# Optimization experiments

Measured on AMD Instinct MI355X. Metric: run time of the kernel, lower is better.

## Reference

```python
import jax, jax.numpy as jnp
import numpy as np

N_USERS = 60000
N_ITEMS = 30000
N_NODES = N_USERS + N_ITEMS
D = 64
L = 2


def _norm_adj(edge_index):
    # symmetrize: A_idx = [e, e.flip(0)]
    src = jnp.concatenate([edge_index[0], edge_index[1]])
    dst = jnp.concatenate([edge_index[1], edge_index[0]])
    ones = jnp.ones_like(src, dtype=jnp.float32)
    deg = jax.ops.segment_sum(ones, src, num_segments=N_NODES)
    deg = jnp.clip(deg, 1.0, None)
    val = jax.lax.rsqrt(deg[src]) * jax.lax.rsqrt(deg[dst])
    return src, dst, val


def _spmm(src, dst, val, x):
    # out[i] = sum_{(i,j) in E} val_ij * x[j]
    return jax.ops.segment_sum(val[:, None] * x[dst], src, num_segments=N_NODES)


def setup_inputs() -> dict:
    key = jax.random.key(0)
    ks = jax.random.split(key, 20)
    s = 0.02
    inp = {
        'x_txt': jax.random.normal(ks[0], (N_ITEMS, 768), jnp.float32),
        'x_img': jax.random.normal(ks[1], (N_ITEMS, 512), jnp.float32),
        'x_struct': jax.random.normal(ks[2], (N_ITEMS, 128), jnp.float32),
        'user_emb': jax.random.normal(ks[3], (3, N_USERS, D), jnp.float32) * s,
        'W_txt': jax.random.normal(ks[4], (3, 768, D), jnp.float32) * s,
        'b_txt': jax.random.normal(ks[5], (3, D), jnp.float32) * s,
        'W_img': jax.random.normal(ks[6], (3, 512, D), jnp.float32) * s,
        'b_img': jax.random.normal(ks[7], (3, D), jnp.float32) * s,
        'W_st': jax.random.normal(ks[8], (3, 128, D), jnp.float32) * s,
        'b_st': jax.random.normal(ks[9], (3, D), jnp.float32) * s,
        'Wu1': jax.random.normal(ks[10], (3 * D, 128), jnp.float32) * s,
        'bu1': jax.random.normal(ks[11], (128,), jnp.float32) * s,
        'Wu2': jax.random.normal(ks[12], (128, 3), jnp.float32) * s,
        'bu2': jax.random.normal(ks[13], (3,), jnp.float32) * s,
        'Wi1': jax.random.normal(ks[14], (3 * D, 128), jnp.float32) * s,
        'bi1': jax.random.normal(ks[15], (128,), jnp.float32) * s,
        'Wi2': jax.random.normal(ks[16], (128, 3), jnp.float32) * s,
        'bi2': jax.random.normal(ks[17], (3,), jnp.float32) * s,
        'edge_index': jax.random.randint(ks[18], (2, 500000), 0, N_NODES, jnp.int64),
    }
    return inp


def reference(x_txt, x_img, x_struct, user_emb, W_txt, b_txt, W_img, b_img,
              W_st, b_st, Wu1, bu1, Wu2, bu2, Wi1, bi1, Wi2, bi2, edge_index):
    src, dst, val = _norm_adj(edge_index)

    # item embeddings for all 3 branches at once: [n_items, 3, d]
    i0 = (jnp.einsum('nt,btd->nbd', x_txt, W_txt) + b_txt
          + jnp.einsum('nt,btd->nbd', x_img, W_img) + b_img
          + jnp.einsum('nt,btd->nbd', x_struct, W_st) + b_st)
    u0 = jnp.transpose(user_emb, (1, 0, 2))  # [n_users, 3, d]
    x = jnp.concatenate([u0, i0], axis=0).reshape(N_NODES, 3 * D)

    out = x
    for _ in range(L):
        x = _spmm(src, dst, val, x)
        out = out + x
    out = out / (L + 1)

    stack = out.reshape(N_NODES, 3, D)
    U_stack, I_stack = stack[:N_USERS], stack[N_USERS:]
    U_cat = U_stack.reshape(N_USERS, 3 * D)
    I_cat = I_stack.reshape(N_ITEMS, 3 * D)

    a_u = jax.nn.softmax(jax.nn.relu(U_cat @ Wu1 + bu1) @ Wu2 + bu2, axis=-1)
    a_i = jax.nn.softmax(jax.nn.relu(I_cat @ Wi1 + bi1) @ Wi2 + bi2, axis=-1)

    U = jnp.einsum('nb,nbd->nd', a_u, U_stack)
    I = jnp.einsum('nb,nbd->nd', a_i, I_stack)
    return jnp.concatenate([U, I], axis=0)  # [N_NODES, d]
```

## Files before the change

### kernel.cpp

```cpp
#include <hip/hip_runtime.h>
#include <math.h>

#define N_USERS 60000
#define N_ITEMS 30000
#define N_NODES 90000
#define DD 64
#define FF 192
#define FH 96
#define KK_TOT 1408
#define E_UND 500000
#define E_DIR 1000000
#define SCAN_NBLK 88

typedef __attribute__((ext_vector_type(8))) __bf16 bf16x8;
typedef __attribute__((ext_vector_type(8))) unsigned short u16x8;
typedef __attribute__((ext_vector_type(4))) float f32x4;

__device__ __forceinline__ unsigned short f2bf(float f) {
    unsigned int u = __float_as_uint(f);
    unsigned int r = (u + 0x7FFFu + ((u >> 16) & 1u)) >> 16;
    return (unsigned short)r;
}
__device__ __forceinline__ float bf_lo(unsigned int x) { return __uint_as_float(x << 16); }
__device__ __forceinline__ float bf_hi(unsigned int x) { return __uint_as_float(x & 0xFFFF0000u); }
__device__ __forceinline__ float bf2f(unsigned short x) {
    return __uint_as_float((unsigned int)x << 16);
}
__device__ __forceinline__ unsigned int pack2(float a, float b) {
    return ((unsigned int)f2bf(b) << 16) | (unsigned int)f2bf(a);
}

__global__ void k_mode(const int* __restrict__ ei, int* __restrict__ mode) {
    __shared__ int any;
    if (threadIdx.x == 0) any = 0;
    __syncthreads();
    if (ei[2 * threadIdx.x + 1] != 0) atomicOr(&any, 1);
    __syncthreads();
    if (threadIdx.x == 0) mode[0] = (any == 0) ? 1 : 0;
}

__device__ __forceinline__ void load_pair(const int* __restrict__ ei, int md, int u,
                                          int& a, int& b) {
    if (md) { a = ei[2 * u]; b = ei[2 * (E_UND + u)]; }
    else    { a = ei[u];     b = ei[E_UND + u]; }
}

__global__ void k_deg(const int* __restrict__ ei, const int* __restrict__ mode,
                      int* __restrict__ deg) {
    int i = blockIdx.x * 256 + threadIdx.x;
    if (i >= E_UND) return;
    int md = mode[0];
    int a, b;
    load_pair(ei, md, i, a, b);
    atomicAdd(&deg[a], 1);
    atomicAdd(&deg[b], 1);
}

__global__ __launch_bounds__(1024) void k_scan1(const int* __restrict__ deg,
                                                int* __restrict__ offs,
                                                int* __restrict__ bsum) {
    __shared__ int tmp[1024];
    int b = blockIdx.x, t = threadIdx.x;
    int i = b * 1024 + t;
    int v = (i < N_NODES) ? deg[i] : 0;
    tmp[t] = v;
    __syncthreads();
    for (int off = 1; off < 1024; off <<= 1) {
        int add = (t >= off) ? tmp[t - off] : 0;
        __syncthreads();
        tmp[t] += add;
        __syncthreads();
    }
    offs[i] = tmp[t] - v;
    if (t == 1023) bsum[b] = tmp[t];
}

__global__ void k_scan2(const int* __restrict__ bsum, int* __restrict__ bscan) {
    if (threadIdx.x == 0) {
        int run = 0;
        for (int b = 0; b < SCAN_NBLK; b++) { bscan[b] = run; run += bsum[b]; }
    }
}

__global__ void k_scan3(const int* __restrict__ deg, int* __restrict__ offs,
                        const int* __restrict__ bscan, int* __restrict__ cursor,
                        float* __restrict__ rsq) {
    int i = blockIdx.x * 256 + threadIdx.x;
    if (i >= N_NODES) return;
    int o = offs[i] + bscan[i >> 10];
    offs[i] = o;
    cursor[i] = o;
    int dg = deg[i];
    if (dg < 1) dg = 1;
    rsq[i] = rsqrtf((float)dg);
}

__global__ void k_fill(const int* __restrict__ ei, const int* __restrict__ mode,
                       int* __restrict__ cursor, const float* __restrict__ rsq,
                       int* __restrict__ edst, float* __restrict__ eval) {
    int i = blockIdx.x * 256 + threadIdx.x;
    if (i >= E_DIR) return;
    int md = mode[0];
    int u = (i < E_UND) ? i : i - E_UND;
    int a, b;
    load_pair(ei, md, u, a, b);
    int s, d;
    if (i < E_UND) { s = a; d = b; } else { s = b; d = a; }
    int slot = atomicAdd(&cursor[s], 1);
    edst[slot] = d;
    eval[slot] = rsq[s] * rsq[d];
}

__global__ void k_users(const float* __restrict__ ue, unsigned short* __restrict__ Xbs) {
    int idx = blockIdx.x * 256 + threadIdx.x;
    if (idx >= N_USERS * FF) return;
    int n = idx / FF;
    int r = idx - n * FF;
    int b = r >> 6, d = r & 63;
    Xbs[idx] = f2bf(ue[((size_t)b * N_USERS + n) * DD + d]);
}

__global__ void k_cvt_w(const float* __restrict__ Wt, const float* __restrict__ Wi,
                        const float* __restrict__ Wst, unsigned short* __restrict__ Wtb) {
    int idx = blockIdx.x * 256 + threadIdx.x;
    if (idx >= FF * KK_TOT) return;
    int n = idx / KK_TOT;
    int k = idx - n * KK_TOT;
    int b = n >> 6, d = n & 63;
    float v;
    if (k < 768)       v = Wt [((size_t)b * 768 + k) * 64 + d];
    else if (k < 1280) v = Wi [((size_t)b * 512 + (k - 768)) * 64 + d];
    else               v = Wst[((size_t)b * 128 + (k - 1280)) * 64 + d];
    Wtb[idx] = f2bf(v);
}

__global__ void k_cvt_w1(const float* __restrict__ Wu1, const float* __restrict__ Wi1,
                         unsigned short* __restrict__ W1Tu,
                         unsigned short* __restrict__ W1Ti) {
    int idx = blockIdx.x * 256 + threadIdx.x;
    if (idx >= 128 * FF) return;
    int n = idx / FF;
    int k = idx - n * FF;
    W1Tu[idx] = f2bf(Wu1[(size_t)k * 128 + n]);
    W1Ti[idx] = f2bf(Wi1[(size_t)k * 128 + n]);
}

#define BM 64
#define BNH 96
#define BK 64
#define LDK 72

__global__ __launch_bounds__(256) void k_item_gemm_mfma3(
    const float* __restrict__ xt, const float* __restrict__ xi, const float* __restrict__ xs,
    const unsigned short* __restrict__ Wtb,
    const float* __restrict__ bt, const float* __restrict__ bi, const float* __restrict__ bst,
    unsigned short* __restrict__ Xbs) {
    __shared__ unsigned short Ash[BM * LDK];
    __shared__ unsigned short Bsh[BNH * LDK];
    const int tid  = threadIdx.x;
    const int wave = tid >> 6;
    const int lane = tid & 63;
    const int row0 = (blockIdx.x >> 1) * BM;
    const int n0   = (blockIdx.x & 1) * BNH;

    f32x4 acc[6];
#pragma unroll
    for (int tn = 0; tn < 6; tn++) acc[tn] = (f32x4){0.f, 0.f, 0.f, 0.f};

    const int l16  = lane & 15;
    const int quad = lane >> 4;

    for (int k0 = 0; k0 < KK_TOT; k0 += BK) {
#pragma unroll
        for (int i = 0; i < 2; i++) {
            int id = tid + i * 256;
            int r = id >> 3;
            int c = (id & 7) << 3;
            int gr = row0 + r;
            int gk = k0 + c;
            float4 v0 = make_float4(0.f, 0.f, 0.f, 0.f);
            float4 v1 = v0;
            if (gr < N_ITEMS) {
                const float* src;
                int kl;
                if (gk < 768)       { src = xt + (size_t)gr * 768; kl = gk; }
                else if (gk < 1280) { src = xi + (size_t)gr * 512; kl = gk - 768; }
                else                { src = xs + (size_t)gr * 128; kl = gk - 1280; }
                v0 = *(const float4*)(src + kl);
                v1 = *(const float4*)(src + kl + 4);
            }
            u16x8 pk;
            pk[0] = f2bf(v0.x); pk[1] = f2bf(v0.y); pk[2] = f2bf(v0.z); pk[3] = f2bf(v0.w);
            pk[4] = f2bf(v1.x); pk[5] = f2bf(v1.y); pk[6] = f2bf(v1.z); pk[7] = f2bf(v1.w);
            *(u16x8*)(&Ash[r * LDK + c]) = pk;
        }
#pragma unroll
        for (int i = 0; i < 3; i++) {
            int id = tid + i * 256;
            int r = id >> 3;
            int c = (id & 7) << 3;
            *(u16x8*)(&Bsh[r * LDK + c]) =
                *(const u16x8*)(&Wtb[(size_t)(n0 + r) * KK_TOT + k0 + c]);
        }
        __syncthreads();
#pragma unroll
        for (int kk = 0; kk < BK; kk += 32) {
            bf16x8 af = *(const bf16x8*)(&Ash[(wave * 16 + l16) * LDK + kk + quad * 8]);
#pragma unroll
            for (int tn = 0; tn < 6; tn++) {
                bf16x8 bfr = *(const bf16x8*)(&Bsh[(tn * 16 + l16) * LDK + kk + quad * 8]);
                acc[tn] = __builtin_amdgcn_mfma_f32_16x16x32_bf16(af, bfr, acc[tn], 0, 0, 0);
            }
        }
        __syncthreads();
    }

#pragma unroll
    for (int tn = 0; tn < 6; tn++) {
        int n = n0 + tn * 16 + l16;
        int b = n >> 6, d = n & 63;
        float bias = bt[b * 64 + d] + bi[b * 64 + d] + bst[b * 64 + d];
#pragma unroll
        for (int r = 0; r < 4; r++) {
            int row = row0 + wave * 16 + quad * 4 + r;
            if (row < N_ITEMS) {
                Xbs[(size_t)(N_USERS + row) * FF + n] = f2bf(acc[tn][r] + bias);
            }
        }
    }
}

__global__ __launch_bounds__(192) void k_spmm_bf(const unsigned int* __restrict__ Xb,
                                                 unsigned int* __restrict__ Yb,
                                                 const int* __restrict__ offs,
                                                 const int* __restrict__ deg,
                                                 const int* __restrict__ edst,
                                                 const float* __restrict__ eval) {
    int t = threadIdx.x;
    int half = (t >= FH) ? 1 : 0;
    int c = t - half * FH;
    int n = blockIdx.x * 2 + half;
    int start = offs[n];
    int dg = deg[n];
    const int* ed = edst + start;
    const float* ev = eval + start;
    float a0 = 0.f, a1 = 0.f;
    for (int j = 0; j < dg; j += 4) {
        int last = dg - 1;
        int j1 = (j + 1 < dg) ? j + 1 : last;
        int j2 = (j + 2 < dg) ? j + 2 : last;
        int j3 = (j + 3 < dg) ? j + 3 : last;
        int d0 = ed[j], d1 = ed[j1], d2 = ed[j2], d3 = ed[j3];
        float v0 = ev[j];
        float v1 = (j + 1 < dg) ? ev[j1] : 0.f;
        float v2 = (j + 2 < dg) ? ev[j2] : 0.f;
        float v3 = (j + 3 < dg) ? ev[j3] : 0.f;
        unsigned int x0 = Xb[(size_t)d0 * FH + c];
        unsigned int x1 = Xb[(size_t)d1 * FH + c];
        unsigned int x2 = Xb[(size_t)d2 * FH + c];
        unsigned int x3 = Xb[(size_t)d3 * FH + c];
        a0 = fmaf(v0, bf_lo(x0), a0); a1 = fmaf(v0, bf_hi(x0), a1);
        a0 = fmaf(v1, bf_lo(x1), a0); a1 = fmaf(v1, bf_hi(x1), a1);
        a0 = fmaf(v2, bf_lo(x2), a0); a1 = fmaf(v2, bf_hi(x2), a1);
        a0 = fmaf(v3, bf_lo(x3), a0); a1 = fmaf(v3, bf_hi(x3), a1);
    }
    Yb[(size_t)n * FH + c] = pack2(a0, a1);
}

#define LDA 200

__global__ __launch_bounds__(256) void k_attn_mfma(
    const unsigned int* __restrict__ X0,
    const unsigned int* __restrict__ X1,
    const unsigned int* __restrict__ X2,
    const unsigned short* __restrict__ W1T,
    const float* __restrict__ B1,
    const float* __restrict__ W2,
    const float* __restrict__ B2,
    float* __restrict__ out,
    int node_base, int n_rows) {
    __shared__ unsigned short Atile[64 * LDA];
    __shared__ float aws[64][4];
    const int tid  = threadIdx.x;
    const int wave = tid >> 6;
    const int lane = tid & 63;
    const int row0 = blockIdx.x * 64;
    const float inv3 = 1.f / 3.f;

#pragma unroll
    for (int i = 0; i < 6; i++) {
        int id = tid + i * 256;
        int r = id / 24;
        int q = id - r * 24;
        u16x8 pk;
        if (row0 + r < n_rows) {
            size_t base = (size_t)(node_base + row0 + r) * FH + q * 4;
            uint4 a = *(const uint4*)(X0 + base);
            uint4 b = *(const uint4*)(X1 + base);
            uint4 c = *(const uint4*)(X2 + base);
            pk[0] = f2bf((bf_lo(a.x) + bf_lo(b.x) + bf_lo(c.x)) * inv3);
            pk[1] = f2bf((bf_hi(a.x) + bf_hi(b.x) + bf_hi(c.x)) * inv3);
            pk[2] = f2bf((bf_lo(a.y) + bf_lo(b.y) + bf_lo(c.y)) * inv3);
            pk[3] = f2bf((bf_hi(a.y) + bf_hi(b.y) + bf_hi(c.y)) * inv3);
            pk[4] = f2bf((bf_lo(a.z) + bf_lo(b.z) + bf_lo(c.z)) * inv3);
            pk[5] = f2bf((bf_hi(a.z) + bf_hi(b.z) + bf_hi(c.z)) * inv3);
            pk[6] = f2bf((bf_lo(a.w) + bf_lo(b.w) + bf_lo(c.w)) * inv3);
            pk[7] = f2bf((bf_hi(a.w) + bf_hi(b.w) + bf_hi(c.w)) * inv3);
        } else {
            pk = (u16x8){0, 0, 0, 0, 0, 0, 0, 0};
        }
        *(u16x8*)(&Atile[r * LDA + q * 8]) = pk;
    }
    __syncthreads();

    f32x4 acc[8];
#pragma unroll
    for (int tn = 0; tn < 8; tn++) acc[tn] = (f32x4){0.f, 0.f, 0.f, 0.f};
    const int l16 = lane & 15;
    const int quad = lane >> 4;
#pragma unroll
    for (int kk = 0; kk < FF; kk += 32) {
        bf16x8 af = *(const bf16x8*)(&Atile[(wave * 16 + l16) * LDA + kk + quad * 8]);
#pragma unroll
        for (int tn = 0; tn < 8; tn++) {
            bf16x8 bf = *(const bf16x8*)(&W1T[(size_t)(tn * 16 + l16) * FF + kk + quad * 8]);
            acc[tn] = __builtin_amdgcn_mfma_f32_16x16x32_bf16(af, bf, acc[tn], 0, 0, 0);
        }
    }

    float pl[4][3];
#pragma unroll
    for (int r = 0; r < 4; r++) { pl[r][0] = 0.f; pl[r][1] = 0.f; pl[r][2] = 0.f; }
#pragma unroll
    for (int tn = 0; tn < 8; tn++) {
        int col = tn * 16 + l16;
        float b1v = B1[col];
        float w0 = W2[col * 3 + 0], w1 = W2[col * 3 + 1], w2v = W2[col * 3 + 2];
#pragma unroll
        for (int r = 0; r < 4; r++) {
            float h = fmaxf(acc[tn][r] + b1v, 0.f);
            pl[r][0] = fmaf(h, w0, pl[r][0]);
            pl[r][1] = fmaf(h, w1, pl[r][1]);
            pl[r][2] = fmaf(h, w2v, pl[r][2]);
        }
    }
#pragma unroll
    for (int m = 1; m <= 8; m <<= 1) {
#pragma unroll
        for (int r = 0; r < 4; r++) {
            pl[r][0] += __shfl_xor(pl[r][0], m, 64);
            pl[r][1] += __shfl_xor(pl[r][1], m, 64);
            pl[r][2] += __shfl_xor(pl[r][2], m, 64);
        }
    }
    float b20 = B2[0], b21 = B2[1], b22 = B2[2];
    if (l16 == 0) {
#pragma unroll
        for (int r = 0; r < 4; r++) {
            float l0 = pl[r][0] + b20, l1 = pl[r][1] + b21, l2 = pl[r][2] + b22;
            float mx = fmaxf(l0, fmaxf(l1, l2));
            float e0 = __expf(l0 - mx), e1 = __expf(l1 - mx), e2 = __expf(l2 - mx);
            float inv = 1.f / (e0 + e1 + e2);
            int rr = wave * 16 + quad * 4 + r;
            aws[rr][0] = e0 * inv; aws[rr][1] = e1 * inv; aws[rr][2] = e2 * inv;
        }
    }
    __syncthreads();

#pragma unroll
    for (int i = 0; i < 16; i++) {
        int flat = tid + i * 256;
        int r = flat >> 6, d = flat & 63;
        if (row0 + r < n_rows) {
            float a0 = aws[r][0], a1 = aws[r][1], a2 = aws[r][2];
            const unsigned short* Ar = &Atile[r * LDA];
            float v = a0 * bf2f(Ar[d]) + a1 * bf2f(Ar[64 + d]) + a2 * bf2f(Ar[128 + d]);
            out[(size_t)(node_base + row0 + r) * DD + d] = v;
        }
    }
}

extern "C" void kernel_launch(void* const* d_in, const int* in_sizes, int n_in,
                              void* d_out, int out_size, void* d_ws, size_t ws_size,
                              hipStream_t stream) {
    (void)in_sizes; (void)n_in; (void)out_size; (void)ws_size;
    const float* x_txt    = (const float*)d_in[0];
    const float* x_img    = (const float*)d_in[1];
    const float* x_struct = (const float*)d_in[2];
    const float* user_emb = (const float*)d_in[3];
    const float* W_txt    = (const float*)d_in[4];
    const float* b_txt    = (const float*)d_in[5];
    const float* W_img    = (const float*)d_in[6];
    const float* b_img    = (const float*)d_in[7];
    const float* W_st     = (const float*)d_in[8];
    const float* b_st     = (const float*)d_in[9];
    const float* Wu1      = (const float*)d_in[10];
    const float* bu1      = (const float*)d_in[11];
    const float* Wu2      = (const float*)d_in[12];
    const float* bu2      = (const float*)d_in[13];
    const float* Wi1      = (const float*)d_in[14];
    const float* bi1      = (const float*)d_in[15];
    const float* Wi2      = (const float*)d_in[16];
    const float* bi2      = (const float*)d_in[17];
    const int*   ei       = (const int*)d_in[18];
    float* out = (float*)d_out;

    char* base = (char*)d_ws;
    size_t off = 0;
    auto take = [&](size_t bytes) -> void* {
        void* p = base + off;
        off += (bytes + 255) & ~(size_t)255;
        return p;
    };
    unsigned int* Xb0  = (unsigned int*)take((size_t)N_NODES * FH * 4);
    unsigned int* Yb   = (unsigned int*)take((size_t)N_NODES * FH * 4);
    unsigned int* Zb   = (unsigned int*)take((size_t)N_NODES * FH * 4);
    int* deg    = (int*)take((size_t)N_NODES * 4);
    int* offs   = (int*)take((size_t)SCAN_NBLK * 1024 * 4);
    int* cursor = (int*)take((size_t)N_NODES * 4);
    int* bsum   = (int*)take((size_t)SCAN_NBLK * 4);
    int* bscan  = (int*)take((size_t)SCAN_NBLK * 4);
    float* rsq  = (float*)take((size_t)N_NODES * 4);
    int* edst   = (int*)take((size_t)E_DIR * 4);
    float* eval = (float*)take((size_t)E_DIR * 4);
    int* mode   = (int*)take(256);
    unsigned short* Wtb  = (unsigned short*)take((size_t)FF * KK_TOT * 2);
    unsigned short* W1Tu = (unsigned short*)take((size_t)128 * FF * 2);
    unsigned short* W1Ti = (unsigned short*)take((size_t)128 * FF * 2);

    hipMemsetAsync(deg, 0, (size_t)N_NODES * 4, stream);

    k_mode<<<1, 256, 0, stream>>>(ei, mode);
    k_deg<<<(E_UND + 255) / 256, 256, 0, stream>>>(ei, mode, deg);
    k_scan1<<<SCAN_NBLK, 1024, 0, stream>>>(deg, offs, bsum);
    k_scan2<<<1, 64, 0, stream>>>(bsum, bscan);
    k_scan3<<<(N_NODES + 255) / 256, 256, 0, stream>>>(deg, offs, bscan, cursor, rsq);
    k_fill<<<(E_DIR + 255) / 256, 256, 0, stream>>>(ei, mode, cursor, rsq, edst, eval);

    k_users<<<(N_USERS * FF + 255) / 256, 256, 0, stream>>>(user_emb,
                                                            (unsigned short*)Xb0);
    k_cvt_w<<<(FF * KK_TOT + 255) / 256, 256, 0, stream>>>(W_txt, W_img, W_st, Wtb);
    k_cvt_w1<<<(128 * FF + 255) / 256, 256, 0, stream>>>(Wu1, Wi1, W1Tu, W1Ti);
    k_item_gemm_mfma3<<<((N_ITEMS + BM - 1) / BM) * 2, 256, 0, stream>>>(
        x_txt, x_img, x_struct, Wtb, b_txt, b_img, b_st, (unsigned short*)Xb0);

    k_spmm_bf<<<N_NODES / 2, 192, 0, stream>>>(Xb0, Yb, offs, deg, edst, eval);
    k_spmm_bf<<<N_NODES / 2, 192, 0, stream>>>(Yb, Zb, offs, deg, edst, eval);

    k_attn_mfma<<<(N_USERS + 63) / 64, 256, 0, stream>>>(
        Xb0, Yb, Zb, W1Tu, bu1, Wu2, bu2, out, 0, N_USERS);
    k_attn_mfma<<<(N_ITEMS + 63) / 64, 256, 0, stream>>>(
        Xb0, Yb, Zb, W1Ti, bi1, Wi2, bi2, out, N_USERS, N_ITEMS);
}
```

Baseline: 619.7 us.

## Double-buffer item GEMM tiles with register prefetch of next K slice

The item-embedding GEMM now keeps two LDS buffers and loads the next K tile's global data into registers while the current tile's MFMAs run. This drops one barrier per iteration and hides global load latency behind compute. Out-of-range rows are clamped to the last row instead of zero-filled, and their outputs are masked at store. The cost is doubled LDS use and more live registers, which may lower occupancy.

```diff
diff --git a/kernel.cpp b/kernel.cpp
--- a/kernel.cpp
+++ b/kernel.cpp
@@ -155,14 +155,43 @@
     const unsigned short* __restrict__ Wtb,
     const float* __restrict__ bt, const float* __restrict__ bi, const float* __restrict__ bst,
     unsigned short* __restrict__ Xbs) {
-    __shared__ unsigned short Ash[BM * LDK];
-    __shared__ unsigned short Bsh[BNH * LDK];
+    __shared__ unsigned short Ash[2][BM * LDK];
+    __shared__ unsigned short Bsh[2][BNH * LDK];
     const int tid  = threadIdx.x;
     const int wave = tid >> 6;
     const int lane = tid & 63;
     const int row0 = (blockIdx.x >> 1) * BM;
     const int n0   = (blockIdx.x & 1) * BNH;
 
+    const int sr = tid >> 3;
+    const int sc = (tid & 7) << 3;
+
+    int gr0 = row0 + sr;        if (gr0 >= N_ITEMS) gr0 = N_ITEMS - 1;
+    int gr1 = row0 + sr + 32;   if (gr1 >= N_ITEMS) gr1 = N_ITEMS - 1;
+
+    const size_t bbase = (size_t)(n0 + sr) * KK_TOT + sc;
+
+    float4 pa[2][2];
+    u16x8  pb[3];
+
+    auto issue = [&](int k0) {
+        int kl = k0 + sc;
+        const float *s0, *s1;
+        if (kl < 768)       { s0 = xt + (size_t)gr0 * 768 + kl;
+                              s1 = xt + (size_t)gr1 * 768 + kl; }
+        else if (kl < 1280) { s0 = xi + (size_t)gr0 * 512 + (kl - 768);
+                              s1 = xi + (size_t)gr1 * 512 + (kl - 768); }
+        else                { s0 = xs + (size_t)gr0 * 128 + (kl - 1280);
+                              s1 = xs + (size_t)gr1 * 128 + (kl - 1280); }
+        pa[0][0] = *(const float4*)(s0);
+        pa[0][1] = *(const float4*)(s0 + 4);
+        pa[1][0] = *(const float4*)(s1);
+        pa[1][1] = *(const float4*)(s1 + 4);
+        pb[0] = *(const u16x8*)(&Wtb[bbase + k0]);
+        pb[1] = *(const u16x8*)(&Wtb[bbase + k0 + (size_t)32 * KK_TOT]);
+        pb[2] = *(const u16x8*)(&Wtb[bbase + k0 + (size_t)64 * KK_TOT]);
+    };
+
     f32x4 acc[6];
 #pragma unroll
     for (int tn = 0; tn < 6; tn++) acc[tn] = (f32x4){0.f, 0.f, 0.f, 0.f};
@@ -170,49 +199,36 @@
     const int l16  = lane & 15;
     const int quad = lane >> 4;
 
+    issue(0);
+    int cur = 0;
     for (int k0 = 0; k0 < KK_TOT; k0 += BK) {
 #pragma unroll
         for (int i = 0; i < 2; i++) {
-            int id = tid + i * 256;
-            int r = id >> 3;
-            int c = (id & 7) << 3;
-            int gr = row0 + r;
-            int gk = k0 + c;
-            float4 v0 = make_float4(0.f, 0.f, 0.f, 0.f);
-            float4 v1 = v0;
-            if (gr < N_ITEMS) {
-                const float* src;
-                int kl;
-                if (gk < 768)       { src = xt + (size_t)gr * 768; kl = gk; }
-                else if (gk < 1280) { src = xi + (size_t)gr * 512; kl = gk - 768; }
-                else                { src = xs + (size_t)gr * 128; kl = gk - 1280; }
-                v0 = *(const float4*)(src + kl);
-                v1 = *(const float4*)(src + kl + 4);
-            }
             u16x8 pk;
-            pk[0] = f2bf(v0.x); pk[1] = f2bf(v0.y); pk[2] = f2bf(v0.z); pk[3] = f2bf(v0.w);
-            pk[4] = f2bf(v1.x); pk[5] = f2bf(v1.y); pk[6] = f2bf(v1.z); pk[7] = f2bf(v1.w);
-            *(u16x8*)(&Ash[r * LDK + c]) = pk;
-        }
-#pragma unroll
-        for (int i = 0; i < 3; i++) {
-            int id = tid + i * 256;
-            int r = id >> 3;
-            int c = (id & 7) << 3;
-            *(u16x8*)(&Bsh[r * LDK + c]) =
-                *(const u16x8*)(&Wtb[(size_t)(n0 + r) * KK_TOT + k0 + c]);
-        }
+            pk[0] = f2bf(pa[i][0].x); pk[1] = f2bf(pa[i][0].y);
+            pk[2] = f2bf(pa[i][0].z); pk[3] = f2bf(pa[i][0].w);
+            pk[4] = f2bf(pa[i][1].x); pk[5] = f2bf(pa[i][1].y);
+            pk[6] = f2bf(pa[i][1].z); pk[7] = f2bf(pa[i][1].w);
+            *(u16x8*)(&Ash[cur][(sr + i * 32) * LDK + sc]) = pk;
+        }
+#pragma unroll
+        for (int i = 0; i < 3; i++)
+            *(u16x8*)(&Bsh[cur][(sr + i * 32) * LDK + sc]) = pb[i];
+
+        if (k0 + BK < KK_TOT) issue(k0 + BK);
+
         __syncthreads();
+
 #pragma unroll
         for (int kk = 0; kk < BK; kk += 32) {
-            bf16x8 af = *(const bf16x8*)(&Ash[(wave * 16 + l16) * LDK + kk + quad * 8]);
+            bf16x8 af = *(const bf16x8*)(&Ash[cur][(wave * 16 + l16) * LDK + kk + quad * 8]);
 #pragma unroll
             for (int tn = 0; tn < 6; tn++) {
-                bf16x8 bfr = *(const bf16x8*)(&Bsh[(tn * 16 + l16) * LDK + kk + quad * 8]);
+                bf16x8 bfr = *(const bf16x8*)(&Bsh[cur][(tn * 16 + l16) * LDK + kk + quad * 8]);
                 acc[tn] = __builtin_amdgcn_mfma_f32_16x16x32_bf16(af, bfr, acc[tn], 0, 0, 0);
             }
         }
-        __syncthreads();
+        cur ^= 1;
     }
 
 #pragma unroll
```

Result: no change. 610.6 us (-1.5%).

## Double-buffer item GEMM with direct global-to-LDS loads and full-N tiles

Applied to the files above, without the earlier changes.

Rewrites the item projection GEMM so each 512-thread block computes all 192 output columns for 64 rows, instead of splitting N across two blocks. That halves the reads of the fp32 activation inputs. Tiles are copied straight into LDS with global_load_lds, using XOR-swizzled layouts and double buffering, so the next K tile loads while MFMAs run on the current one. The fp32-to-bf16 conversion moves from the staging path to fragment-read time. The cost is more LDS per block, repeated conversions, and hand-placed waitcnt and barrier synchronisation that must be exactly right.

```diff
diff --git a/kernel.cpp b/kernel.cpp
--- a/kernel.cpp
+++ b/kernel.cpp
@@ -15,6 +15,18 @@
 typedef __attribute__((ext_vector_type(8))) __bf16 bf16x8;
 typedef __attribute__((ext_vector_type(8))) unsigned short u16x8;
 typedef __attribute__((ext_vector_type(4))) float f32x4;
+
+typedef __attribute__((address_space(1))) const void gvoid;
+typedef __attribute__((address_space(3))) void svoid;
+
+__device__ __forceinline__ void gll16(const void* g, void* l) {
+    __builtin_amdgcn_global_load_lds((gvoid*)g, (svoid*)l, 16, 0, 0);
+}
+__device__ __forceinline__ void fence_bar() {
+    asm volatile("" ::: "memory");
+    __builtin_amdgcn_s_barrier();
+    asm volatile("" ::: "memory");
+}
 
 __device__ __forceinline__ unsigned short f2bf(float f) {
     unsigned int u = __float_as_uint(f);
@@ -146,83 +158,100 @@
 }
 
 #define BM 64
-#define BNH 96
 #define BK 64
-#define LDK 72
-
-__global__ __launch_bounds__(256) void k_item_gemm_mfma3(
+#define NT (KK_TOT / BK)
+
+__global__ __launch_bounds__(512, 4) void k_item_gemm_mfma3(
     const float* __restrict__ xt, const float* __restrict__ xi, const float* __restrict__ xs,
     const unsigned short* __restrict__ Wtb,
     const float* __restrict__ bt, const float* __restrict__ bi, const float* __restrict__ bst,
     unsigned short* __restrict__ Xbs) {
-    __shared__ unsigned short Ash[BM * LDK];
-    __shared__ unsigned short Bsh[BNH * LDK];
+    __shared__ float          Ashf[2][BM * BK];
+    __shared__ unsigned short Bsh [2][FF * BK];
     const int tid  = threadIdx.x;
-    const int wave = tid >> 6;
+    const int w    = tid >> 6;
     const int lane = tid & 63;
-    const int row0 = (blockIdx.x >> 1) * BM;
-    const int n0   = (blockIdx.x & 1) * BNH;
-
-    f32x4 acc[6];
-#pragma unroll
-    for (int tn = 0; tn < 6; tn++) acc[tn] = (f32x4){0.f, 0.f, 0.f, 0.f};
-
+    const int row0 = blockIdx.x * BM;
     const int l16  = lane & 15;
     const int quad = lane >> 4;
-
-    for (int k0 = 0; k0 < KK_TOT; k0 += BK) {
+    const int rg   = w & 3;
+    const int ng   = w >> 2;
+
+    const int ac = lane & 15;
+    const int bc = lane & 7;
+
+    auto stage = [&](int k0, int buf) {
 #pragma unroll
         for (int i = 0; i < 2; i++) {
-            int id = tid + i * 256;
-            int r = id >> 3;
-            int c = (id & 7) << 3;
-            int gr = row0 + r;
-            int gk = k0 + c;
-            float4 v0 = make_float4(0.f, 0.f, 0.f, 0.f);
-            float4 v1 = v0;
-            if (gr < N_ITEMS) {
-                const float* src;
-                int kl;
-                if (gk < 768)       { src = xt + (size_t)gr * 768; kl = gk; }
-                else if (gk < 1280) { src = xi + (size_t)gr * 512; kl = gk - 768; }
-                else                { src = xs + (size_t)gr * 128; kl = gk - 1280; }
-                v0 = *(const float4*)(src + kl);
-                v1 = *(const float4*)(src + kl + 4);
+            int rb = w * 8 + i * 4;
+            int r  = rb + (lane >> 4);
+            int gr = row0 + r; if (gr >= N_ITEMS) gr = N_ITEMS - 1;
+            const float* rp;
+            if (k0 < 768)       rp = xt + (size_t)gr * 768 + k0;
+            else if (k0 < 1280) rp = xi + (size_t)gr * 512 + (k0 - 768);
+            else                rp = xs + (size_t)gr * 128 + (k0 - 1280);
+            gll16(rp + ((ac ^ (r & 15)) << 2), &Ashf[buf][rb * BK]);
+        }
+#pragma unroll
+        for (int j = 0; j < 3; j++) {
+            int rb = w * 24 + j * 8;
+            int r  = rb + (lane >> 3);
+            gll16(Wtb + (size_t)r * KK_TOT + k0 + ((bc ^ (r & 7)) << 3),
+                  &Bsh[buf][rb * BK]);
+        }
+    };
+
+    f32x4 acc[6];
+#pragma unroll
+    for (int tn = 0; tn < 6; tn++) acc[tn] = (f32x4){0.f, 0.f, 0.f, 0.f};
+
+    auto compute = [&](int buf) {
+#pragma unroll
+        for (int kk = 0; kk < BK; kk += 32) {
+            const int rA = rg * 16 + l16;
+            const float* Ab = &Ashf[buf][rA * BK];
+            const int c0 = (kk >> 2) + quad * 2;
+            float4 a0 = *(const float4*)(Ab + (((c0    ) ^ l16) << 2));
+            float4 a1 = *(const float4*)(Ab + (((c0 + 1) ^ l16) << 2));
+            bf16x8 af;
+            af[0] = (__bf16)a0.x; af[1] = (__bf16)a0.y;
+            af[2] = (__bf16)a0.z; af[3] = (__bf16)a0.w;
+            af[4] = (__bf16)a1.x; af[5] = (__bf16)a1.y;
+            af[6] = (__bf16)a1.z; af[7] = (__bf16)a1.w;
+            const int cB = (kk >> 3) + quad;
+#pragma unroll
+            for (int tn = 0; tn < 6; tn++) {
+                int R = ng * 96 + tn * 16 + l16;
+                bf16x8 bfrag = *(const bf16x8*)(&Bsh[buf][R * BK + ((cB ^ (R & 7)) << 3)]);
+                acc[tn] = __builtin_amdgcn_mfma_f32_16x16x32_bf16(af, bfrag, acc[tn], 0, 0, 0);
             }
-            u16x8 pk;
-            pk[0] = f2bf(v0.x); pk[1] = f2bf(v0.y); pk[2] = f2bf(v0.z); pk[3] = f2bf(v0.w);
-            pk[4] = f2bf(v1.x); pk[5] = f2bf(v1.y); pk[6] = f2bf(v1.z); pk[7] = f2bf(v1.w);
-            *(u16x8*)(&Ash[r * LDK + c]) = pk;
-        }
-#pragma unroll
-        for (int i = 0; i < 3; i++) {
-            int id = tid + i * 256;
-            int r = id >> 3;
-            int c = (id & 7) << 3;
-            *(u16x8*)(&Bsh[r * LDK + c]) =
-                *(const u16x8*)(&Wtb[(size_t)(n0 + r) * KK_TOT + k0 + c]);
-        }
-        __syncthreads();
-#pragma unroll
-        for (int kk = 0; kk < BK; kk += 32) {
-            bf16x8 af = *(const bf16x8*)(&Ash[(wave * 16 + l16) * LDK + kk + quad * 8]);
-#pragma unroll
-            for (int tn = 0; tn < 6; tn++) {
-                bf16x8 bfr = *(const bf16x8*)(&Bsh[(tn * 16 + l16) * LDK + kk + quad * 8]);
-                acc[tn] = __builtin_amdgcn_mfma_f32_16x16x32_bf16(af, bfr, acc[tn], 0, 0, 0);
-            }
-        }
-        __syncthreads();
-    }
+        }
+    };
+
+    stage(0, 0);
+    int cur = 0;
+#pragma unroll 1
+    for (int t = 0; t < NT - 1; ++t) {
+        fence_bar();
+        stage((t + 1) * BK, cur ^ 1);
+        asm volatile("s_waitcnt vmcnt(5)" ::: "memory");
+        fence_bar();
+        compute(cur);
+        cur ^= 1;
+    }
+    fence_bar();
+    asm volatile("s_waitcnt vmcnt(0)" ::: "memory");
+    fence_bar();
+    compute(cur);
 
 #pragma unroll
     for (int tn = 0; tn < 6; tn++) {
-        int n = n0 + tn * 16 + l16;
+        int n = ng * 96 + tn * 16 + l16;
         int b = n >> 6, d = n & 63;
         float bias = bt[b * 64 + d] + bi[b * 64 + d] + bst[b * 64 + d];
 #pragma unroll
         for (int r = 0; r < 4; r++) {
-            int row = row0 + wave * 16 + quad * 4 + r;
+            int row = row0 + rg * 16 + quad * 4 + r;
             if (row < N_ITEMS) {
                 Xbs[(size_t)(N_USERS + row) * FF + n] = f2bf(acc[tn][r] + bias);
             }
@@ -441,7 +470,7 @@
                                                             (unsigned short*)Xb0);
     k_cvt_w<<<(FF * KK_TOT + 255) / 256, 256, 0, stream>>>(W_txt, W_img, W_st, Wtb);
     k_cvt_w1<<<(128 * FF + 255) / 256, 256, 0, stream>>>(Wu1, Wi1, W1Tu, W1Ti);
-    k_item_gemm_mfma3<<<((N_ITEMS + BM - 1) / BM) * 2, 256, 0, stream>>>(
+    k_item_gemm_mfma3<<<(N_ITEMS + BM - 1) / BM, 512, 0, stream>>>(
         x_txt, x_img, x_struct, Wtb, b_txt, b_img, b_st, (unsigned short*)Xb0);
 
     k_spmm_bf<<<N_NODES / 2, 192, 0, stream>>>(Xb0, Yb, offs, deg, edst, eval);
```

Result: faster. 604.4 us (-2.5%).

## Register-pipelined item GEMM without LDS; compute edge weights from per-node rsqrt

Applied to the files above, without the earlier changes.

The item projection GEMM drops its shared-memory staging. Each wave now loads A rows (fp32, converted to bf16 in registers) and B fragments straight from global memory, with a multi-stage software prefetch, using 384-thread blocks over 32 rows that cover all 192 output columns. Separately, the per-edge value array is removed. The SpMM multiplies by rsq[dst] per edge and by rsq[src] once per row, which saves the fill-time multiply and the eval stream write and read. The trade-off is an extra random gather of rsq per edge, and B fragments that every block re-reads from global memory or cache instead of sharing them through LDS.

```diff
diff --git a/kernel.cpp b/kernel.cpp
--- a/kernel.cpp
+++ b/kernel.cpp
@@ -96,8 +96,8 @@
 }
 
 __global__ void k_fill(const int* __restrict__ ei, const int* __restrict__ mode,
-                       int* __restrict__ cursor, const float* __restrict__ rsq,
-                       int* __restrict__ edst, float* __restrict__ eval) {
+                       int* __restrict__ cursor,
+                       int* __restrict__ edst) {
     int i = blockIdx.x * 256 + threadIdx.x;
     if (i >= E_DIR) return;
     int md = mode[0];
@@ -108,7 +108,6 @@
     if (i < E_UND) { s = a; d = b; } else { s = b; d = a; }
     int slot = atomicAdd(&cursor[s], 1);
     edst[slot] = d;
-    eval[slot] = rsq[s] * rsq[d];
 }
 
 __global__ void k_users(const float* __restrict__ ue, unsigned short* __restrict__ Xbs) {
@@ -145,84 +144,96 @@
     W1Ti[idx] = f2bf(Wi1[(size_t)k * 128 + n]);
 }
 
-#define BM 64
-#define BNH 96
-#define BK 64
-#define LDK 72
-
-__global__ __launch_bounds__(256) void k_item_gemm_mfma3(
+#define BM 32
+#define NTT (KK_TOT / 64)
+
+__global__ __launch_bounds__(384, 4) void k_item_gemm_reg(
     const float* __restrict__ xt, const float* __restrict__ xi, const float* __restrict__ xs,
     const unsigned short* __restrict__ Wtb,
     const float* __restrict__ bt, const float* __restrict__ bi, const float* __restrict__ bst,
     unsigned short* __restrict__ Xbs) {
-    __shared__ unsigned short Ash[BM * LDK];
-    __shared__ unsigned short Bsh[BNH * LDK];
     const int tid  = threadIdx.x;
-    const int wave = tid >> 6;
+    const int w    = tid >> 6;
     const int lane = tid & 63;
-    const int row0 = (blockIdx.x >> 1) * BM;
-    const int n0   = (blockIdx.x & 1) * BNH;
-
-    f32x4 acc[6];
-#pragma unroll
-    for (int tn = 0; tn < 6; tn++) acc[tn] = (f32x4){0.f, 0.f, 0.f, 0.f};
-
     const int l16  = lane & 15;
     const int quad = lane >> 4;
-
-    for (int k0 = 0; k0 < KK_TOT; k0 += BK) {
-#pragma unroll
-        for (int i = 0; i < 2; i++) {
-            int id = tid + i * 256;
-            int r = id >> 3;
-            int c = (id & 7) << 3;
-            int gr = row0 + r;
-            int gk = k0 + c;
-            float4 v0 = make_float4(0.f, 0.f, 0.f, 0.f);
-            float4 v1 = v0;
-            if (gr < N_ITEMS) {
-                const float* src;
-                int kl;
-                if (gk < 768)       { src = xt + (size_t)gr * 768; kl = gk; }
-                else if (gk < 1280) { src = xi + (size_t)gr * 512; kl = gk - 768; }
-                else                { src = xs + (size_t)gr * 128; kl = gk - 1280; }
-                v0 = *(const float4*)(src + kl);
-                v1 = *(const float4*)(src + kl + 4);
-            }
-            u16x8 pk;
-            pk[0] = f2bf(v0.x); pk[1] = f2bf(v0.y); pk[2] = f2bf(v0.z); pk[3] = f2bf(v0.w);
-            pk[4] = f2bf(v1.x); pk[5] = f2bf(v1.y); pk[6] = f2bf(v1.z); pk[7] = f2bf(v1.w);
-            *(u16x8*)(&Ash[r * LDK + c]) = pk;
-        }
-#pragma unroll
-        for (int i = 0; i < 3; i++) {
-            int id = tid + i * 256;
-            int r = id >> 3;
-            int c = (id & 7) << 3;
-            *(u16x8*)(&Bsh[r * LDK + c]) =
-                *(const u16x8*)(&Wtb[(size_t)(n0 + r) * KK_TOT + k0 + c]);
-        }
-        __syncthreads();
-#pragma unroll
-        for (int kk = 0; kk < BK; kk += 32) {
-            bf16x8 af = *(const bf16x8*)(&Ash[(wave * 16 + l16) * LDK + kk + quad * 8]);
-#pragma unroll
-            for (int tn = 0; tn < 6; tn++) {
-                bf16x8 bfr = *(const bf16x8*)(&Bsh[(tn * 16 + l16) * LDK + kk + quad * 8]);
-                acc[tn] = __builtin_amdgcn_mfma_f32_16x16x32_bf16(af, bfr, acc[tn], 0, 0, 0);
-            }
-        }
-        __syncthreads();
-    }
-
-#pragma unroll
-    for (int tn = 0; tn < 6; tn++) {
-        int n = n0 + tn * 16 + l16;
+    const int rg   = w & 1;
+    const int ng   = w >> 1;
+    const int row0 = blockIdx.x * BM;
+
+    int gr = row0 + rg * 16 + l16;
+    if (gr >= N_ITEMS) gr = N_ITEMS - 1;
+
+    const float* at  = xt + (size_t)gr * 768 + quad * 8;
+    const float* ai  = xi + (size_t)gr * 512 + quad * 8;
+    const float* as_ = xs + (size_t)gr * 128 + quad * 8;
+
+    const unsigned short* bb0 = Wtb + (size_t)(ng * 64 +  0 + l16) * KK_TOT + quad * 8;
+    const unsigned short* bb1 = Wtb + (size_t)(ng * 64 + 16 + l16) * KK_TOT + quad * 8;
+    const unsigned short* bb2 = Wtb + (size_t)(ng * 64 + 32 + l16) * KK_TOT + quad * 8;
+    const unsigned short* bb3 = Wtb + (size_t)(ng * 64 + 48 + l16) * KK_TOT + quad * 8;
+
+    f32x4 acc[4];
+#pragma unroll
+    for (int tn = 0; tn < 4; tn++) acc[tn] = (f32x4){0.f, 0.f, 0.f, 0.f};
+
+    float4 A[3][2][2];
+    bf16x8 Bf[2][4];
+
+    auto loadA = [&](int t, int st) {
+#pragma unroll
+        for (int h = 0; h < 2; h++) {
+            int kb = t * 64 + h * 32;
+            const float* p;
+            if (kb < 768)       p = at  + kb;
+            else if (kb < 1280) p = ai  + (kb - 768);
+            else                p = as_ + (kb - 1280);
+            A[st][h][0] = *(const float4*)(p);
+            A[st][h][1] = *(const float4*)(p + 4);
+        }
+    };
+    auto loadB = [&](int h, int bs) {
+        int kb = (h >> 1) * 64 + (h & 1) * 32;
+        Bf[bs][0] = *(const bf16x8*)(bb0 + kb);
+        Bf[bs][1] = *(const bf16x8*)(bb1 + kb);
+        Bf[bs][2] = *(const bf16x8*)(bb2 + kb);
+        Bf[bs][3] = *(const bf16x8*)(bb3 + kb);
+    };
+
+    loadA(0, 0);
+    loadB(0, 0);
+    loadA(1, 1);
+
+#pragma unroll
+    for (int t = 0; t < NTT; t++) {
+        const int as3 = t % 3;
+#pragma unroll
+        for (int h2 = 0; h2 < 2; h2++) {
+            const int h  = 2 * t + h2;
+            const int bs = h & 1;
+            if (h + 1 < 2 * NTT) loadB(h + 1, bs ^ 1);
+            if (h2 == 0 && t + 2 < NTT) loadA(t + 2, (t + 2) % 3);
+            float4 a0 = A[as3][h2][0];
+            float4 a1 = A[as3][h2][1];
+            bf16x8 af;
+            af[0] = (__bf16)a0.x; af[1] = (__bf16)a0.y;
+            af[2] = (__bf16)a0.z; af[3] = (__bf16)a0.w;
+            af[4] = (__bf16)a1.x; af[5] = (__bf16)a1.y;
+            af[6] = (__bf16)a1.z; af[7] = (__bf16)a1.w;
+#pragma unroll
+            for (int tn = 0; tn < 4; tn++)
+                acc[tn] = __builtin_amdgcn_mfma_f32_16x16x32_bf16(af, Bf[bs][tn], acc[tn], 0, 0, 0);
+        }
+    }
+
+#pragma unroll
+    for (int tn = 0; tn < 4; tn++) {
+        int n = ng * 64 + tn * 16 + l16;
         int b = n >> 6, d = n & 63;
         float bias = bt[b * 64 + d] + bi[b * 64 + d] + bst[b * 64 + d];
 #pragma unroll
         for (int r = 0; r < 4; r++) {
-            int row = row0 + wave * 16 + quad * 4 + r;
+            int row = row0 + rg * 16 + quad * 4 + r;
             if (row < N_ITEMS) {
                 Xbs[(size_t)(N_USERS + row) * FF + n] = f2bf(acc[tn][r] + bias);
             }
@@ -235,7 +246,7 @@
                                                  const int* __restrict__ offs,
                                                  const int* __restrict__ deg,
                                                  const int* __restrict__ edst,
-                                                 const float* __restrict__ eval) {
+                                                 const float* __restrict__ rsq) {
     int t = threadIdx.x;
     int half = (t >= FH) ? 1 : 0;
     int c = t - half * FH;
@@ -243,7 +254,6 @@
     int start = offs[n];
     int dg = deg[n];
     const int* ed = edst + start;
-    const float* ev = eval + start;
     float a0 = 0.f, a1 = 0.f;
     for (int j = 0; j < dg; j += 4) {
         int last = dg - 1;
@@ -251,10 +261,10 @@
         int j2 = (j + 2 < dg) ? j + 2 : last;
         int j3 = (j + 3 < dg) ? j + 3 : last;
         int d0 = ed[j], d1 = ed[j1], d2 = ed[j2], d3 = ed[j3];
-        float v0 = ev[j];
-        float v1 = (j + 1 < dg) ? ev[j1] : 0.f;
-        float v2 = (j + 2 < dg) ? ev[j2] : 0.f;
-        float v3 = (j + 3 < dg) ? ev[j3] : 0.f;
+        float v0 = rsq[d0];
+        float v1 = (j + 1 < dg) ? rsq[d1] : 0.f;
+        float v2 = (j + 2 < dg) ? rsq[d2] : 0.f;
+        float v3 = (j + 3 < dg) ? rsq[d3] : 0.f;
         unsigned int x0 = Xb[(size_t)d0 * FH + c];
         unsigned int x1 = Xb[(size_t)d1 * FH + c];
         unsigned int x2 = Xb[(size_t)d2 * FH + c];
@@ -264,7 +274,8 @@
         a0 = fmaf(v2, bf_lo(x2), a0); a1 = fmaf(v2, bf_hi(x2), a1);
         a0 = fmaf(v3, bf_lo(x3), a0); a1 = fmaf(v3, bf_hi(x3), a1);
     }
-    Yb[(size_t)n * FH + c] = pack2(a0, a1);
+    float rs = rsq[n];
+    Yb[(size_t)n * FH + c] = pack2(a0 * rs, a1 * rs);
 }
 
 #define LDA 200
@@ -422,7 +433,6 @@
     int* bscan  = (int*)take((size_t)SCAN_NBLK * 4);
     float* rsq  = (float*)take((size_t)N_NODES * 4);
     int* edst   = (int*)take((size_t)E_DIR * 4);
-    float* eval = (float*)take((size_t)E_DIR * 4);
     int* mode   = (int*)take(256);
     unsigned short* Wtb  = (unsigned short*)take((size_t)FF * KK_TOT * 2);
     unsigned short* W1Tu = (unsigned short*)take((size_t)128 * FF * 2);
@@ -435,17 +445,17 @@
     k_scan1<<<SCAN_NBLK, 1024, 0, stream>>>(deg, offs, bsum);
     k_scan2<<<1, 64, 0, stream>>>(bsum, bscan);
     k_scan3<<<(N_NODES + 255) / 256, 256, 0, stream>>>(deg, offs, bscan, cursor, rsq);
-    k_fill<<<(E_DIR + 255) / 256, 256, 0, stream>>>(ei, mode, cursor, rsq, edst, eval);
+    k_fill<<<(E_DIR + 255) / 256, 256, 0, stream>>>(ei, mode, cursor, edst);
 
     k_users<<<(N_USERS * FF + 255) / 256, 256, 0, stream>>>(user_emb,
                                                             (unsigned short*)Xb0);
     k_cvt_w<<<(FF * KK_TOT + 255) / 256, 256, 0, stream>>>(W_txt, W_img, W_st, Wtb);
     k_cvt_w1<<<(128 * FF + 255) / 256, 256, 0, stream>>>(Wu1, Wi1, W1Tu, W1Ti);
-    k_item_gemm_mfma3<<<((N_ITEMS + BM - 1) / BM) * 2, 256, 0, stream>>>(
+    k_item_gemm_reg<<<(N_ITEMS + BM - 1) / BM, 384, 0, stream>>>(
         x_txt, x_img, x_struct, Wtb, b_txt, b_img, b_st, (unsigned short*)Xb0);
 
-    k_spmm_bf<<<N_NODES / 2, 192, 0, stream>>>(Xb0, Yb, offs, deg, edst, eval);
-    k_spmm_bf<<<N_NODES / 2, 192, 0, stream>>>(Yb, Zb, offs, deg, edst, eval);
+    k_spmm_bf<<<N_NODES / 2, 192, 0, stream>>>(Xb0, Yb, offs, deg, edst, rsq);
+    k_spmm_bf<<<N_NODES / 2, 192, 0, stream>>>(Yb, Zb, offs, deg, edst, rsq);
 
     k_attn_mfma<<<(N_USERS + 63) / 64, 256, 0, stream>>>(
         Xb0, Yb, Zb, W1Tu, bu1, Wu2, bu2, out, 0, N_USERS);
```

Result: slower. 793.3 us (+28.0%).
